# Performance work log

Measured on AMD Instinct MI355X. Metric: run time of the kernel, lower is better.

The kernel has to match this reference:

```python
import jax, jax.numpy as jnp
import numpy as np

FP4_VALUES = jnp.array([0.0, 0.5, 1.0, 1.5, 2.0, 3.0, 4.0, 6.0,
                        -0.0, -0.5, -1.0, -1.5, -2.0, -3.0, -4.0, -6.0], dtype=jnp.float32)
ALPHA = 1.702   # swiglu alpha
LIMIT = 7.0     # swiglu clamp limit
TOP_K = 4       # experts per token
EPS = 1e-5      # rmsnorm eps


def dequant_mxfp4(blocks, scales):
    """blocks: [E, R, G, B] int (uint8 values), scales: [E, R, G] int (E8M0 biased exp).
    Returns decoded weights [E, R, G*2B] fp32. Low nibble -> even cols, high nibble -> odd."""
    lo = FP4_VALUES[blocks & 15]
    hi = FP4_VALUES[(blocks >> 4) & 15]
    vals = jnp.stack([lo, hi], axis=-1).reshape(blocks.shape[:-1] + (-1,))  # [E,R,G,2B]
    w = jnp.ldexp(vals, (scales - 127)[..., None])
    return w.reshape(blocks.shape[:-2] + (-1,))


def rmsnorm(x, w):
    return x * jax.lax.rsqrt(jnp.mean(x * x, axis=-1, keepdims=True) + EPS) * w


def setup_inputs():
    key = jax.random.key(0)
    ks = jax.random.split(key, 10)
    E, H, I, B, S = 32, 1024, 1024, 1, 1024
    GB = 16  # packed bytes per 32-element group
    return {
        "x": jax.random.normal(ks[0], (B, S, H), jnp.float32),
        "norm_w": jnp.ones((H,), jnp.float32),
        "gate_w": jax.random.normal(ks[1], (E, H), jnp.float32) * 0.05,
        "gate_b": jax.random.normal(ks[2], (E,), jnp.float32) * 0.01,
        "mlp1_bias": jax.random.normal(ks[3], (E, 2 * I), jnp.float32) * 0.02,
        "mlp2_bias": jax.random.normal(ks[4], (E, H), jnp.float32) * 0.02,
        "mlp1_blocks": jax.random.randint(ks[5], (E, 2 * I, H // 32, GB), 0, 256, jnp.int32),
        "mlp1_scales": jax.random.randint(ks[6], (E, 2 * I, H // 32), 118, 125, jnp.int32),
        "mlp2_blocks": jax.random.randint(ks[7], (E, H, I // 32, GB), 0, 256, jnp.int32),
        "mlp2_scales": jax.random.randint(ks[8], (E, H, I // 32), 118, 125, jnp.int32),
    }


def reference(x, norm_w, gate_w, gate_b, mlp1_bias, mlp2_bias,
              mlp1_blocks, mlp1_scales, mlp2_blocks, mlp2_scales):
    B, S, H = x.shape
    N = B * S
    E = gate_w.shape[0]

    t = rmsnorm(x, norm_w).reshape(N, H)
    logits = t @ gate_w.T + gate_b                      # [N, E]
    top_vals, top_idx = jax.lax.top_k(logits, TOP_K)     # sorted descending, like torch.topk
    top_w = jax.nn.softmax(top_vals, axis=-1)            # [N, K]
    # dense routing matrix: nonzero only at selected experts (indices unique per token)
    route = jnp.zeros((N, E), x.dtype).at[jnp.arange(N)[:, None], top_idx].add(top_w)

    w1 = dequant_mxfp4(mlp1_blocks, mlp1_scales)         # [E, 2I, H]
    w2 = dequant_mxfp4(mlp2_blocks, mlp2_scales)         # [E, H, I]

    h = jnp.einsum('nh,eih->nei', t, w1) + mlp1_bias[None]  # [N, E, 2I]
    x_glu = jnp.minimum(h[..., 0::2], LIMIT)
    x_lin = jnp.clip(h[..., 1::2], -LIMIT, LIMIT)
    a = x_glu * jax.nn.sigmoid(ALPHA * x_glu) * (x_lin + 1.0)   # [N, E, I]
    y = jnp.einsum('nei,ehi->neh', a, w2) + mlp2_bias[None]      # [N, E, H]
    out = jnp.einsum('neh,ne->nh', y, route)                     # weighted combine
    return x + out.reshape(B, S, H)
```

## Files before the change

kernel.cpp:

```cpp
#include <hip/hip_runtime.h>
#include <hip/hip_bf16.h>
#include <math.h>


#define NE 32
#define HD 1024
#define ID 1024
#define NTOK 1024
#define R1 2048
#define TCH 160

typedef __attribute__((ext_vector_type(8)))  short bf16x8;
typedef __attribute__((ext_vector_type(16))) float f32x16;

#define TB_OFF   0
#define A_OFF    2097152
#define YB_OFF   10485760
#define CNT_OFF  18874368
#define OFFS_OFF 18874624
#define TOKL_OFF 18874880
#define TIDX_OFF 19005952
#define TWT_OFF  19022336
#define POS_OFF  19038720

__device__ __forceinline__ unsigned f2bf(float f) {
    unsigned u = __float_as_uint(f);
    return (u + 0x7FFFu + ((u >> 16) & 1u)) >> 16;
}
__device__ __forceinline__ float bf2f(unsigned u) {
    return __uint_as_float(u << 16);
}

__device__ __forceinline__ void dec8(int4 wv, unsigned dd, uint4& o) {
    unsigned u = __builtin_amdgcn_perm((unsigned)wv.y, (unsigned)wv.x, 0x00000400u);
    unsigned v = __builtin_amdgcn_perm((unsigned)wv.w, (unsigned)wv.z, 0x04000000u);
    unsigned packed = __builtin_amdgcn_perm(v, u, 0x07060100u);
    unsigned selE = packed & 0x07070707u;
    unsigned sE   = packed & 0x08080808u;
    unsigned ph   = packed >> 4;
    unsigned selO = ph & 0x07070707u;
    unsigned sO   = ph & 0x08080808u;
    const unsigned PH_hi = 0x40404040u, PH_lo = 0x3F3F3F14u;
    const unsigned PL_hi = 0xC0804000u, PL_lo = 0xC0800000u;
    unsigned hbE = __builtin_amdgcn_perm(PH_hi, PH_lo, selE) | (sE << 4);
    unsigned lbE = __builtin_amdgcn_perm(PL_hi, PL_lo, selE);
    unsigned hbO = __builtin_amdgcn_perm(PH_hi, PH_lo, selO) | (sO << 4);
    unsigned lbO = __builtin_amdgcn_perm(PL_hi, PL_lo, selO);
    unsigned mE0 = __builtin_amdgcn_perm(hbE, lbE, 0x05010400u);
    unsigned mE1 = __builtin_amdgcn_perm(hbE, lbE, 0x07030602u);
    unsigned mO0 = __builtin_amdgcn_perm(hbO, lbO, 0x05010400u);
    unsigned mO1 = __builtin_amdgcn_perm(hbO, lbO, 0x07030602u);
    unsigned r0 = __builtin_amdgcn_perm(mO0, mE0, 0x05040100u);
    unsigned r1 = __builtin_amdgcn_perm(mO0, mE0, 0x07060302u);
    unsigned r2 = __builtin_amdgcn_perm(mO1, mE1, 0x05040100u);
    unsigned r3 = __builtin_amdgcn_perm(mO1, mE1, 0x07060302u);
    unsigned o0, o1, o2, o3;
    asm("v_pk_add_u16 %0, %1, %2" : "=v"(o0) : "v"(r0), "v"(dd));
    asm("v_pk_add_u16 %0, %1, %2" : "=v"(o1) : "v"(r1), "v"(dd));
    asm("v_pk_add_u16 %0, %1, %2" : "=v"(o2) : "v"(r2), "v"(dd));
    asm("v_pk_add_u16 %0, %1, %2" : "=v"(o3) : "v"(r3), "v"(dd));
    o.x = o0; o.y = o1; o.z = o2; o.w = o3;
}

__global__ __launch_bounds__(256) void k_gate(
    const float* __restrict__ x, const float* __restrict__ norm_w,
    const float* __restrict__ gate_w, const float* __restrict__ gate_b,
    ushort* __restrict__ t_bf16, int* __restrict__ top_idx, float* __restrict__ top_wt)
{
    int n = blockIdx.x;
    int tid = threadIdx.x;
    __shared__ float tl[HD];
    __shared__ float red[4];
    __shared__ float logits[NE];

    const float4* xv = (const float4*)(x + (size_t)n * HD);
    float4 v = xv[tid];
    float ss = v.x * v.x + v.y * v.y + v.z * v.z + v.w * v.w;
    #pragma unroll
    for (int off = 32; off; off >>= 1) ss += __shfl_down(ss, off);
    if ((tid & 63) == 0) red[tid >> 6] = ss;
    __syncthreads();
    float tot = red[0] + red[1] + red[2] + red[3];
    float rms = rsqrtf(tot * (1.0f / HD) + 1e-5f);

    float4 w = ((const float4*)norm_w)[tid];
    float4 tv;
    tv.x = v.x * rms * w.x; tv.y = v.y * rms * w.y;
    tv.z = v.z * rms * w.z; tv.w = v.w * rms * w.w;
    ushort4 tb;
    tb.x = (ushort)f2bf(tv.x); tb.y = (ushort)f2bf(tv.y);
    tb.z = (ushort)f2bf(tv.z); tb.w = (ushort)f2bf(tv.w);
    ((ushort4*)(t_bf16 + (size_t)n * HD))[tid] = tb;
    ((float4*)tl)[tid] = tv;
    __syncthreads();

    int wv = tid >> 6, lane = tid & 63;
    for (int j = 0; j < 8; j++) {
        int e = wv * 8 + j;
        const float* gw = gate_w + (size_t)e * HD;
        float p = 0.f;
        #pragma unroll
        for (int q = 0; q < 16; q++) { int kk = lane + q * 64; p += tl[kk] * gw[kk]; }
        #pragma unroll
        for (int off = 32; off; off >>= 1) p += __shfl_down(p, off);
        if (lane == 0) logits[e] = p + gate_b[e];
    }
    __syncthreads();

    if (tid == 0) {
        float vals[4]; int idx[4];
        unsigned used = 0;
        #pragma unroll
        for (int kk = 0; kk < 4; kk++) {
            float best = -1e30f; int bi = 0;
            for (int e2 = 0; e2 < NE; e2++) {
                if (used & (1u << e2)) continue;
                if (logits[e2] > best) { best = logits[e2]; bi = e2; }
            }
            used |= 1u << bi; vals[kk] = best; idx[kk] = bi;
        }
        float m = vals[0], s = 0.f, ex[4];
        #pragma unroll
        for (int kk = 0; kk < 4; kk++) { ex[kk] = __expf(vals[kk] - m); s += ex[kk]; }
        float inv = 1.0f / s;
        #pragma unroll
        for (int kk = 0; kk < 4; kk++) {
            top_idx[n * 4 + kk] = idx[kk];
            top_wt[n * 4 + kk] = ex[kk] * inv;
        }
    }
}

__global__ void k_build(const int* __restrict__ top_idx, int* __restrict__ counts,
                        int* __restrict__ tok_list, int* __restrict__ pos_of)
{
    int i = blockIdx.x * 256 + threadIdx.x;
    if (i >= NTOK * 4) return;
    int n = i >> 2;
    int e = top_idx[i];
    int slot = atomicAdd(counts + e, 1);
    tok_list[e * NTOK + slot] = n;
    pos_of[i] = slot;
}

__global__ void k_prefix(const int* __restrict__ counts, int* __restrict__ offsets)
{
    if (threadIdx.x == 0) {
        int s = 0;
        for (int e = 0; e < NE; e++) { offsets[e] = s; s += counts[e]; }
        offsets[NE] = s;
    }
}

__global__ __launch_bounds__(256) void k_mlp1(
    const ushort* __restrict__ t_bf16, const int* __restrict__ blocks,
    const int* __restrict__ scales, const float* __restrict__ bias,
    const int* __restrict__ counts, const int* __restrict__ offsets,
    const int* __restrict__ tok_list, ushort* __restrict__ a)
{
    int e = blockIdx.y;
    int cnt = counts[e];
    if (cnt == 0) return;
    int r0 = blockIdx.x * 128;
    int tid = threadIdx.x;
    int w = tid >> 6, l = tid & 63;
    int base = offsets[e];

    __shared__ ushort tl[TCH][72];
    __shared__ ushort wl[128][72];
    __shared__ int tlist[TCH];

    int lrow = r0 + w * 32 + (l & 31);
    float b_lane = bias[e * R1 + lrow];
    int srow = tid >> 1, shalf = tid & 1;

    for (int c0 = 0; c0 < cnt; c0 += TCH) {
        int nt = min(TCH, cnt - c0);
        __syncthreads();
        if (tid < TCH) tlist[tid] = tok_list[e * NTOK + c0 + min(tid, nt - 1)];
        f32x16 acc[5] = {};

        #pragma unroll 1
        for (int k0 = 0; k0 < HD; k0 += 64) {
            __syncthreads();
            for (int idx = tid; idx < TCH * 8; idx += 256) {
                int tok = idx >> 3, seg = idx & 7;
                *(uint4*)&tl[tok][seg * 8] =
                    *(const uint4*)(t_bf16 + (size_t)tlist[tok] * HD + k0 + seg * 8);
            }
            {
                int g = (k0 >> 5) + shalf;
                size_t rbase = (size_t)(e * R1 + r0 + srow) * 32 + g;
                int s = scales[rbase];
                unsigned dd16 = (unsigned)((s - 127) << 7) & 0xFFFFu;
                unsigned dd = dd16 | (dd16 << 16);
                const int4* wp = (const int4*)(blocks + rbase * 16);
                ushort* dst = &wl[srow][shalf * 32];
                #pragma unroll
                for (int q = 0; q < 4; q++) {
                    uint4 ov;
                    dec8(wp[q], dd, ov);
                    *(uint4*)(dst + q * 8) = ov;
                }
            }
            __syncthreads();
            #pragma unroll
            for (int ks = 0; ks < 4; ks++) {
                bf16x8 wf = *(const bf16x8*)&wl[w * 32 + (l & 31)][ks * 16 + (l >> 5) * 8];
                #pragma unroll
                for (int mt = 0; mt < 5; mt++) {
                    bf16x8 af = *(const bf16x8*)&tl[mt * 32 + (l & 31)][ks * 16 + (l >> 5) * 8];
                    acc[mt] = __builtin_amdgcn_mfma_f32_32x32x16_bf16(af, wf, acc[mt], 0, 0, 0);
                }
            }
        }

        int p0 = (r0 + w * 32) >> 1;
        int pcol = p0 + ((l & 31) >> 1);
        #pragma unroll
        for (int mt = 0; mt < 5; mt++) {
            #pragma unroll
            for (int r = 0; r < 16; r++) {
                float h = acc[mt][r] + b_lane;
                float other = __shfl_xor(h, 1, 64);
                int m = (r & 3) + 8 * (r >> 2) + 4 * (l >> 5);
                int tokg = c0 + mt * 32 + m;
                if (!(l & 1) && tokg < cnt) {
                    float hg = fminf(h, 7.0f);
                    float hx = fminf(fmaxf(other, -7.0f), 7.0f);
                    float sig = 1.0f / (1.0f + __expf(-1.702f * hg));
                    float av = hg * sig * (hx + 1.0f);
                    a[(size_t)(base + tokg) * ID + pcol] = (ushort)f2bf(av);
                }
            }
        }
    }
}

__global__ __launch_bounds__(256) void k_mlp2(
    const ushort* __restrict__ a, const int* __restrict__ blocks,
    const int* __restrict__ scales, const float* __restrict__ bias,
    const int* __restrict__ counts, const int* __restrict__ offsets,
    ushort* __restrict__ yb)
{
    int e = blockIdx.y;
    int cnt = counts[e];
    if (cnt == 0) return;
    int r0 = blockIdx.x * 128;
    int tid = threadIdx.x;
    int w = tid >> 6, l = tid & 63;
    int base = offsets[e];

    __shared__ ushort tl[TCH][72];
    __shared__ ushort wl[128][72];

    int lrow = r0 + w * 32 + (l & 31);
    float b_lane = bias[e * HD + lrow];
    int srow = tid >> 1, shalf = tid & 1;

    for (int c0 = 0; c0 < cnt; c0 += TCH) {
        int nt = min(TCH, cnt - c0);
        f32x16 acc[5] = {};

        #pragma unroll 1
        for (int k0 = 0; k0 < ID; k0 += 64) {
            __syncthreads();
            for (int idx = tid; idx < TCH * 8; idx += 256) {
                int tok = idx >> 3, seg = idx & 7;
                int slot = base + c0 + min(tok, nt - 1);
                *(uint4*)&tl[tok][seg * 8] =
                    *(const uint4*)(a + (size_t)slot * ID + k0 + seg * 8);
            }
            {
                int g = (k0 >> 5) + shalf;
                size_t rbase = (size_t)(e * HD + r0 + srow) * 32 + g;
                int s = scales[rbase];
                unsigned dd16 = (unsigned)((s - 127) << 7) & 0xFFFFu;
                unsigned dd = dd16 | (dd16 << 16);
                const int4* wp = (const int4*)(blocks + rbase * 16);
                ushort* dst = &wl[srow][shalf * 32];
                #pragma unroll
                for (int q = 0; q < 4; q++) {
                    uint4 ov;
                    dec8(wp[q], dd, ov);
                    *(uint4*)(dst + q * 8) = ov;
                }
            }
            __syncthreads();
            #pragma unroll
            for (int ks = 0; ks < 4; ks++) {
                bf16x8 wf = *(const bf16x8*)&wl[w * 32 + (l & 31)][ks * 16 + (l >> 5) * 8];
                #pragma unroll
                for (int mt = 0; mt < 5; mt++) {
                    bf16x8 af = *(const bf16x8*)&tl[mt * 32 + (l & 31)][ks * 16 + (l >> 5) * 8];
                    acc[mt] = __builtin_amdgcn_mfma_f32_32x32x16_bf16(af, wf, acc[mt], 0, 0, 0);
                }
            }
        }

        int hcol = r0 + w * 32 + (l & 31);
        #pragma unroll
        for (int mt = 0; mt < 5; mt++) {
            #pragma unroll
            for (int r = 0; r < 16; r++) {
                int m = (r & 3) + 8 * (r >> 2) + 4 * (l >> 5);
                int tokg = c0 + mt * 32 + m;
                if (tokg < cnt) {
                    float y = acc[mt][r] + b_lane;
                    yb[(size_t)(base + tokg) * HD + hcol] = (ushort)f2bf(y);
                }
            }
        }
    }
}

__global__ __launch_bounds__(256) void k_combine(
    const float* __restrict__ x, const ushort* __restrict__ yb,
    const int* __restrict__ top_idx, const float* __restrict__ top_wt,
    const int* __restrict__ pos_of, const int* __restrict__ offsets,
    float* __restrict__ out)
{
    int n = blockIdx.x, tid = threadIdx.x;
    float4 xv = ((const float4*)(x + (size_t)n * HD))[tid];
    float r0 = xv.x, r1 = xv.y, r2 = xv.z, r3 = xv.w;
    #pragma unroll
    for (int k = 0; k < 4; k++) {
        int e = top_idx[n * 4 + k];
        float wt = top_wt[n * 4 + k];
        int slot = offsets[e] + pos_of[n * 4 + k];
        ushort4 yv = ((const ushort4*)(yb + (size_t)slot * HD))[tid];
        r0 += wt * bf2f(yv.x); r1 += wt * bf2f(yv.y);
        r2 += wt * bf2f(yv.z); r3 += wt * bf2f(yv.w);
    }
    float4 ov; ov.x = r0; ov.y = r1; ov.z = r2; ov.w = r3;
    ((float4*)(out + (size_t)n * HD))[tid] = ov;
}

extern "C" void kernel_launch(void* const* d_in, const int* in_sizes, int n_in,
                              void* d_out, int out_size, void* d_ws, size_t ws_size,
                              hipStream_t stream)
{
    const float* x           = (const float*)d_in[0];
    const float* norm_w      = (const float*)d_in[1];
    const float* gate_w      = (const float*)d_in[2];
    const float* gate_b      = (const float*)d_in[3];
    const float* mlp1_bias   = (const float*)d_in[4];
    const float* mlp2_bias   = (const float*)d_in[5];
    const int*   mlp1_blocks = (const int*)d_in[6];
    const int*   mlp1_scales = (const int*)d_in[7];
    const int*   mlp2_blocks = (const int*)d_in[8];
    const int*   mlp2_scales = (const int*)d_in[9];
    float* out = (float*)d_out;

    char* ws = (char*)d_ws;
    ushort* t_bf16  = (ushort*)(ws + TB_OFF);
    ushort* a       = (ushort*)(ws + A_OFF);
    ushort* yb      = (ushort*)(ws + YB_OFF);
    int*   counts   = (int*)(ws + CNT_OFF);
    int*   offsets  = (int*)(ws + OFFS_OFF);
    int*   tok_list = (int*)(ws + TOKL_OFF);
    int*   top_idx  = (int*)(ws + TIDX_OFF);
    float* top_wt   = (float*)(ws + TWT_OFF);
    int*   pos_of   = (int*)(ws + POS_OFF);

    hipMemsetAsync(counts, 0, NE * sizeof(int), stream);
    k_gate<<<NTOK, 256, 0, stream>>>(x, norm_w, gate_w, gate_b, t_bf16, top_idx, top_wt);
    k_build<<<(NTOK * 4 + 255) / 256, 256, 0, stream>>>(top_idx, counts, tok_list, pos_of);
    k_prefix<<<1, 64, 0, stream>>>(counts, offsets);
    k_mlp1<<<dim3(16, NE), 256, 0, stream>>>(t_bf16, mlp1_blocks, mlp1_scales, mlp1_bias,
                                             counts, offsets, tok_list, a);
    k_mlp2<<<dim3(8, NE), 256, 0, stream>>>(a, mlp2_blocks, mlp2_scales, mlp2_bias,
                                            counts, offsets, yb);
    k_combine<<<NTOK, 256, 0, stream>>>(x, yb, top_idx, top_wt, pos_of, offsets, out);
}
```

Measured before the change: 153.8 us.

## Repack MXFP4 weights, fold routing into gate, pipeline MLPs with direct-to-LDS loads

Adds a repack kernel that compacts the int32-stored fp4 blocks and scales into dense swizzled layouts each call. The gate kernel now assigns expert slots itself and scatters activations into a fixed per-expert, K-tiled layout, which removes the build and prefix kernels. Both MLP kernels are rewritten to use per-wave global_load_lds double buffering with manual waitcnt scheduling, register-held scales, 2x2 MFMA tiles and a split over token chunks via a grid z dimension. The repack pass adds traffic over the full weight set on every call, and the workspace grows considerably.

```diff
diff --git a/kernel.cpp b/kernel.cpp
--- a/kernel.cpp
+++ b/kernel.cpp
@@ -8,20 +8,23 @@
 #define ID 1024
 #define NTOK 1024
 #define R1 2048
-#define TCH 160
+#define SLOTS 32768
+#define TSTEP 4194304
 
 typedef __attribute__((ext_vector_type(8)))  short bf16x8;
 typedef __attribute__((ext_vector_type(16))) float f32x16;
 
-#define TB_OFF   0
-#define A_OFF    2097152
-#define YB_OFF   10485760
-#define CNT_OFF  18874368
-#define OFFS_OFF 18874624
-#define TOKL_OFF 18874880
-#define TIDX_OFF 19005952
-#define TWT_OFF  19022336
-#define POS_OFF  19038720
+#define WP1_OFF  0
+#define WP2_OFF  33554432
+#define SCT1_OFF 50331648
+#define SCT2_OFF 52428800
+#define TS_OFF   53477376
+#define AK_OFF   120586240
+#define YB_OFF   187695104
+#define CNT_OFF  254803968
+#define TIDX_OFF 254804224
+#define TWT_OFF  254820608
+#define POS_OFF  254836992
 
 __device__ __forceinline__ unsigned f2bf(float f) {
     unsigned u = __float_as_uint(f);
@@ -31,10 +34,7 @@
     return __uint_as_float(u << 16);
 }
 
-__device__ __forceinline__ void dec8(int4 wv, unsigned dd, uint4& o) {
-    unsigned u = __builtin_amdgcn_perm((unsigned)wv.y, (unsigned)wv.x, 0x00000400u);
-    unsigned v = __builtin_amdgcn_perm((unsigned)wv.w, (unsigned)wv.z, 0x04000000u);
-    unsigned packed = __builtin_amdgcn_perm(v, u, 0x07060100u);
+__device__ __forceinline__ bf16x8 dec8p(unsigned packed, unsigned dd) {
     unsigned selE = packed & 0x07070707u;
     unsigned sE   = packed & 0x08080808u;
     unsigned ph   = packed >> 4;
@@ -59,19 +59,103 @@
     asm("v_pk_add_u16 %0, %1, %2" : "=v"(o1) : "v"(r1), "v"(dd));
     asm("v_pk_add_u16 %0, %1, %2" : "=v"(o2) : "v"(r2), "v"(dd));
     asm("v_pk_add_u16 %0, %1, %2" : "=v"(o3) : "v"(r3), "v"(dd));
-    o.x = o0; o.y = o1; o.z = o2; o.w = o3;
+    uint4 o; o.x = o0; o.y = o1; o.z = o2; o.w = o3;
+    union { uint4 u4; bf16x8 b; } cv; cv.u4 = o;
+    return cv.b;
+}
+
+__device__ __forceinline__ void gll16(const void* g, void* l) {
+    __builtin_amdgcn_global_load_lds(
+        (const __attribute__((address_space(1))) unsigned int*)g,
+        (__attribute__((address_space(3))) unsigned int*)l, 16, 0, 0);
+}
+
+#define SB __builtin_amdgcn_sched_barrier(0)
+
+__device__ __forceinline__ unsigned sc_sel(uint4 a, uint4 b, int kt2) {
+    int idx = kt2 >> 1;
+    unsigned r0_ = (idx & 4) ? b.x : a.x;
+    unsigned r1_ = (idx & 4) ? b.y : a.y;
+    unsigned r2_ = (idx & 4) ? b.z : a.z;
+    unsigned r3_ = (idx & 4) ? b.w : a.w;
+    unsigned lo = (idx & 1) ? r1_ : r0_;
+    unsigned hi = (idx & 1) ? r3_ : r2_;
+    return (idx & 2) ? hi : lo;
+}
+
+__device__ __forceinline__ void repack_w_item(const int* __restrict__ blocks,
+                                              unsigned* __restrict__ wp, int rsh, int idx)
+{
+    int R = 1 << rsh;
+    int row = idx & (R - 1);
+    int ekt = idx >> rsh;
+    const int4* src = (const int4*)(blocks + ((size_t)(ekt >> 4) * R + row) * 512
+                                    + (ekt & 15) * 32);
+    unsigned d[8];
+    #pragma unroll
+    for (int q = 0; q < 8; q++) {
+        int4 v = src[q];
+        unsigned u = __builtin_amdgcn_perm((unsigned)v.y, (unsigned)v.x, 0x00000400u);
+        unsigned w = __builtin_amdgcn_perm((unsigned)v.w, (unsigned)v.z, 0x04000000u);
+        d[q] = __builtin_amdgcn_perm(w, u, 0x07060100u);
+    }
+    int r63 = row & 63;
+    int x = (r63 ^ (r63 >> 3)) & 7;
+    unsigned t;
+    if (x & 1) { t=d[0];d[0]=d[1];d[1]=t; t=d[2];d[2]=d[3];d[3]=t;
+                 t=d[4];d[4]=d[5];d[5]=t; t=d[6];d[6]=d[7];d[7]=t; }
+    if (x & 2) { t=d[0];d[0]=d[2];d[2]=t; t=d[1];d[1]=d[3];d[3]=t;
+                 t=d[4];d[4]=d[6];d[6]=t; t=d[5];d[5]=d[7];d[7]=t; }
+    if (x & 4) { t=d[0];d[0]=d[4];d[4]=t; t=d[1];d[1]=d[5];d[5]=t;
+                 t=d[2];d[2]=d[6];d[6]=t; t=d[3];d[3]=d[7];d[7]=t; }
+    uint4 o0; o0.x=d[0]; o0.y=d[1]; o0.z=d[2]; o0.w=d[3];
+    uint4 o1; o1.x=d[4]; o1.y=d[5]; o1.z=d[6]; o1.w=d[7];
+    *(uint4*)(wp + (size_t)idx * 8) = o0;
+    *(uint4*)(wp + (size_t)idx * 8 + 4) = o1;
+}
+
+__device__ __forceinline__ void repack_sc_item(const int* __restrict__ scales,
+                                               ushort* __restrict__ sct, int idx)
+{
+    const int* src = scales + (size_t)idx * 32;
+    unsigned o[8];
+    #pragma unroll
+    for (int d = 0; d < 8; d++) {
+        unsigned w0 = (src[4*d] & 0xFF) | ((src[4*d+1] & 0xFF) << 8);
+        unsigned w1 = (src[4*d+2] & 0xFF) | ((src[4*d+3] & 0xFF) << 8);
+        o[d] = w0 | (w1 << 16);
+    }
+    uint4 a; a.x=o[0]; a.y=o[1]; a.z=o[2]; a.w=o[3];
+    uint4 b; b.x=o[4]; b.y=o[5]; b.z=o[6]; b.w=o[7];
+    *(uint4*)(sct + (size_t)idx * 16) = a;
+    *(uint4*)(sct + (size_t)idx * 16 + 8) = b;
+}
+
+__global__ __launch_bounds__(256) void k_repack(
+    const int* __restrict__ b1, const int* __restrict__ b2,
+    const int* __restrict__ s1, const int* __restrict__ s2,
+    unsigned* __restrict__ wp1, unsigned* __restrict__ wp2,
+    ushort* __restrict__ sct1, ushort* __restrict__ sct2)
+{
+    int b = blockIdx.x, tid = threadIdx.x;
+    if (b < 4096)       repack_w_item(b1, wp1, 11, b * 256 + tid);
+    else if (b < 6144)  repack_w_item(b2, wp2, 10, (b - 4096) * 256 + tid);
+    else if (b < 6400)  repack_sc_item(s1, sct1, (b - 6144) * 256 + tid);
+    else                repack_sc_item(s2, sct2, (b - 6400) * 256 + tid);
 }
 
 __global__ __launch_bounds__(256) void k_gate(
     const float* __restrict__ x, const float* __restrict__ norm_w,
     const float* __restrict__ gate_w, const float* __restrict__ gate_b,
-    ushort* __restrict__ t_bf16, int* __restrict__ top_idx, float* __restrict__ top_wt)
+    ushort* __restrict__ t_s, int* __restrict__ top_idx, float* __restrict__ top_wt,
+    int* __restrict__ counts, int* __restrict__ pos_of)
 {
     int n = blockIdx.x;
     int tid = threadIdx.x;
     __shared__ float tl[HD];
     __shared__ float red[4];
     __shared__ float logits[NE];
+    __shared__ int s_se[4], s_sl[4];
 
     const float4* xv = (const float4*)(x + (size_t)n * HD);
     float4 v = xv[tid];
@@ -90,7 +174,6 @@
     ushort4 tb;
     tb.x = (ushort)f2bf(tv.x); tb.y = (ushort)f2bf(tv.y);
     tb.z = (ushort)f2bf(tv.z); tb.w = (ushort)f2bf(tv.w);
-    ((ushort4*)(t_bf16 + (size_t)n * HD))[tid] = tb;
     ((float4*)tl)[tid] = tv;
     __syncthreads();
 
@@ -127,198 +210,256 @@
         for (int kk = 0; kk < 4; kk++) {
             top_idx[n * 4 + kk] = idx[kk];
             top_wt[n * 4 + kk] = ex[kk] * inv;
+            int slot = atomicAdd(counts + idx[kk], 1);
+            pos_of[n * 4 + kk] = slot;
+            s_se[kk] = idx[kk]; s_sl[kk] = slot;
         }
     }
-}
-
-__global__ void k_build(const int* __restrict__ top_idx, int* __restrict__ counts,
-                        int* __restrict__ tok_list, int* __restrict__ pos_of)
-{
-    int i = blockIdx.x * 256 + threadIdx.x;
-    if (i >= NTOK * 4) return;
-    int n = i >> 2;
-    int e = top_idx[i];
-    int slot = atomicAdd(counts + e, 1);
-    tok_list[e * NTOK + slot] = n;
-    pos_of[i] = slot;
-}
-
-__global__ void k_prefix(const int* __restrict__ counts, int* __restrict__ offsets)
-{
-    if (threadIdx.x == 0) {
-        int s = 0;
-        for (int e = 0; e < NE; e++) { offsets[e] = s; s += counts[e]; }
-        offsets[NE] = s;
-    }
-}
-
-__global__ __launch_bounds__(256) void k_mlp1(
-    const ushort* __restrict__ t_bf16, const int* __restrict__ blocks,
-    const int* __restrict__ scales, const float* __restrict__ bias,
-    const int* __restrict__ counts, const int* __restrict__ offsets,
-    const int* __restrict__ tok_list, ushort* __restrict__ a)
+    __syncthreads();
+
+    int kt = tid >> 4, off = (tid & 15) * 4;
+    #pragma unroll
+    for (int kk = 0; kk < 4; kk++) {
+        int slot = (s_se[kk] << 10) + s_sl[kk];
+        *(ushort4*)&t_s[((size_t)kt * SLOTS + slot) * 64 + off] = tb;
+    }
+}
+
+#define M1_ISSUE(buf, kt) {                                                   \
+    const char* ws_ = wsrc + (size_t)(kt) * 65536;                            \
+    gll16(ws_, myw + (buf) * 2048);                                           \
+    gll16(ws_ + 1024, myw + (buf) * 2048 + 1024);                             \
+    const char* ts_ = tsrc + (size_t)(kt) * TSTEP;                            \
+    _Pragma("unroll")                                                         \
+    for (int i_ = 0; i_ < 8; i_++)                                            \
+        gll16(ts_ + i_ * 1024, myt + (buf) * 8192 + i_ * 1024);               \
+}
+
+#define M1_COMPUTE(buf, wordA, wordB) {                                       \
+    unsigned wa_ = (wordA), wb_ = (wordB);                                    \
+    unsigned dAl = (unsigned)(((int)(wa_ & 0xFF) - 127) << 7) & 0xFFFFu; dAl |= dAl << 16; \
+    unsigned dAh = (unsigned)(((int)((wa_ >> 8) & 0xFF) - 127) << 7) & 0xFFFFu; dAh |= dAh << 16; \
+    unsigned dBl = (unsigned)(((int)(wb_ & 0xFF) - 127) << 7) & 0xFFFFu; dBl |= dBl << 16; \
+    unsigned dBh = (unsigned)(((int)((wb_ >> 8) & 0xFF) - 127) << 7) & 0xFFFFu; dBh |= dBh << 16; \
+    _Pragma("unroll")                                                         \
+    for (int ks = 0; ks < 4; ks++) {                                          \
+        int s_ = ks * 2 + kh;                                                 \
+        unsigned w0_ = *(const unsigned*)(myw + (buf) * 2048 + lr * 32 + ((s_ ^ swz0) << 2)); \
+        unsigned w1_ = *(const unsigned*)(myw + (buf) * 2048 + (32 + lr) * 32 + ((s_ ^ swz1) << 2)); \
+        bf16x8 wf0 = dec8p(w0_, ks < 2 ? dAl : dAh);                          \
+        bf16x8 wf1 = dec8p(w1_, ks < 2 ? dBl : dBh);                          \
+        bf16x8 af0 = *(const bf16x8*)(myt + (buf) * 8192 + lr * 128 + ((s_ ^ (lr & 7)) << 4)); \
+        bf16x8 af1 = *(const bf16x8*)(myt + (buf) * 8192 + (32 + lr) * 128 + ((s_ ^ (lr & 7)) << 4)); \
+        a00 = __builtin_amdgcn_mfma_f32_32x32x16_bf16(af0, wf0, a00, 0, 0, 0); \
+        a01 = __builtin_amdgcn_mfma_f32_32x32x16_bf16(af1, wf0, a01, 0, 0, 0); \
+        a10 = __builtin_amdgcn_mfma_f32_32x32x16_bf16(af0, wf1, a10, 0, 0, 0); \
+        a11 = __builtin_amdgcn_mfma_f32_32x32x16_bf16(af1, wf1, a11, 0, 0, 0); \
+    }                                                                         \
+}
+
+#define M1_EPI(ac, nn, mt) {                                                  \
+    float bl = (nn) ? blB : blA;                                              \
+    int row_ = (nn) ? rowB : rowA;                                            \
+    int cc = (row_ >> 1) & 63;                                                \
+    _Pragma("unroll")                                                         \
+    for (int r = 0; r < 16; r++) {                                            \
+        float hv = ac[r] + bl;                                                \
+        float other = __shfl_xor(hv, 1, 64);                                  \
+        int m = (r & 3) + 8 * (r >> 2) + 4 * kh;                              \
+        int tokg = c0 + wt * 64 + (mt) * 32 + m;                              \
+        if (!(l & 1) && tokg < cnt) {                                         \
+            float hg = fminf(hv, 7.0f);                                       \
+            float hx = fminf(fmaxf(other, -7.0f), 7.0f);                      \
+            float sig = 1.0f / (1.0f + __expf(-1.702f * hg));                 \
+            float av = hg * sig * (hx + 1.0f);                                \
+            a_k[((size_t)g0 * SLOTS + sbase + tokg) * 64 + cc] = (ushort)f2bf(av); \
+        }                                                                     \
+    }                                                                         \
+}
+
+__global__ __launch_bounds__(256, 2) void k_mlp1(
+    const ushort* __restrict__ t_s, const unsigned* __restrict__ wp,
+    const ushort* __restrict__ sct, const float* __restrict__ bias,
+    const int* __restrict__ counts, ushort* __restrict__ a_k)
 {
     int e = blockIdx.y;
     int cnt = counts[e];
     if (cnt == 0) return;
+    int c00 = blockIdx.z * 128;
+    if (c00 >= cnt) return;
     int r0 = blockIdx.x * 128;
     int tid = threadIdx.x;
-    int w = tid >> 6, l = tid & 63;
-    int base = offsets[e];
-
-    __shared__ ushort tl[TCH][72];
-    __shared__ ushort wl[128][72];
-    __shared__ int tlist[TCH];
-
-    int lrow = r0 + w * 32 + (l & 31);
-    float b_lane = bias[e * R1 + lrow];
-    int srow = tid >> 1, shalf = tid & 1;
-
-    for (int c0 = 0; c0 < cnt; c0 += TCH) {
-        int nt = min(TCH, cnt - c0);
-        __syncthreads();
-        if (tid < TCH) tlist[tid] = tok_list[e * NTOK + c0 + min(tid, nt - 1)];
-        f32x16 acc[5] = {};
+    int l = tid & 63, lr = l & 31, kh = l >> 5;
+    int wu = __builtin_amdgcn_readfirstlane(tid >> 6);
+    int wr = wu >> 1, wt = wu & 1;
+    int sbase = e << 10;
+    int g0 = r0 >> 7;
+
+    __shared__ char lds_all[81920];
+    char* myt = lds_all + wu * 20480;
+    char* myw = myt + 16384;
+
+    int rowA = r0 + wr * 64 + lr, rowB = rowA + 32;
+    float blA = bias[e * R1 + rowA];
+    float blB = bias[e * R1 + rowB];
+    const uint4* spA = (const uint4*)(sct + (size_t)(e * R1 + rowA) * 16);
+    const uint4* spB = (const uint4*)(sct + (size_t)(e * R1 + rowB) * 16);
+    uint4 sA0 = spA[0], sA1 = spA[1];
+    uint4 sB0 = spB[0], sB1 = spB[1];
+    unsigned pin = sA0.x ^ sA0.y ^ sA0.z ^ sA0.w ^ sA1.x ^ sA1.y ^ sA1.z ^ sA1.w
+                 ^ sB0.x ^ sB0.y ^ sB0.z ^ sB0.w ^ sB1.x ^ sB1.y ^ sB1.z ^ sB1.w;
+    asm volatile("" :: "v"(pin), "v"(blA), "v"(blB));
+
+    const char* wsrc = (const char*)wp + (size_t)e * 16 * 65536
+                       + (size_t)(r0 + wr * 64) * 32 + (l >> 1) * 32 + (l & 1) * 16;
+    int tswz = ((l & 7) ^ (l >> 3)) << 4;
+    int swz0 = (lr ^ (lr >> 3)) & 7;
+    int swz1 = swz0 ^ 4;
+
+    #pragma unroll 1
+    for (int c0 = c00; c0 < cnt; c0 += 256) {
+        const char* tsrc = (const char*)t_s
+            + (size_t)(sbase + c0 + wt * 64 + (l >> 3)) * 128 + tswz;
+        asm volatile("s_waitcnt vmcnt(0)" ::: "memory"); SB;
+
+        f32x16 a00 = {}, a01 = {}, a10 = {}, a11 = {};
+        M1_ISSUE(0, 0); M1_ISSUE(1, 1); SB;
 
         #pragma unroll 1
-        for (int k0 = 0; k0 < HD; k0 += 64) {
-            __syncthreads();
-            for (int idx = tid; idx < TCH * 8; idx += 256) {
-                int tok = idx >> 3, seg = idx & 7;
-                *(uint4*)&tl[tok][seg * 8] =
-                    *(const uint4*)(t_bf16 + (size_t)tlist[tok] * HD + k0 + seg * 8);
-            }
-            {
-                int g = (k0 >> 5) + shalf;
-                size_t rbase = (size_t)(e * R1 + r0 + srow) * 32 + g;
-                int s = scales[rbase];
-                unsigned dd16 = (unsigned)((s - 127) << 7) & 0xFFFFu;
-                unsigned dd = dd16 | (dd16 << 16);
-                const int4* wp = (const int4*)(blocks + rbase * 16);
-                ushort* dst = &wl[srow][shalf * 32];
-                #pragma unroll
-                for (int q = 0; q < 4; q++) {
-                    uint4 ov;
-                    dec8(wp[q], dd, ov);
-                    *(uint4*)(dst + q * 8) = ov;
-                }
-            }
-            __syncthreads();
-            #pragma unroll
-            for (int ks = 0; ks < 4; ks++) {
-                bf16x8 wf = *(const bf16x8*)&wl[w * 32 + (l & 31)][ks * 16 + (l >> 5) * 8];
-                #pragma unroll
-                for (int mt = 0; mt < 5; mt++) {
-                    bf16x8 af = *(const bf16x8*)&tl[mt * 32 + (l & 31)][ks * 16 + (l >> 5) * 8];
-                    acc[mt] = __builtin_amdgcn_mfma_f32_32x32x16_bf16(af, wf, acc[mt], 0, 0, 0);
-                }
-            }
+        for (int kt2 = 0; kt2 < 16; kt2 += 2) {
+            unsigned dwA = sc_sel(sA0, sA1, kt2);
+            unsigned dwB = sc_sel(sB0, sB1, kt2);
+            asm volatile("s_waitcnt vmcnt(10)" ::: "memory"); SB;
+            M1_COMPUTE(0, dwA & 0xFFFFu, dwB & 0xFFFFu);
+            asm volatile("s_waitcnt lgkmcnt(0)" ::: "memory"); SB;
+            if (kt2 < 14) { M1_ISSUE(0, kt2 + 2); SB; }
+            if (kt2 < 14) { asm volatile("s_waitcnt vmcnt(10)" ::: "memory"); }
+            else          { asm volatile("s_waitcnt vmcnt(0)" ::: "memory"); }
+            SB;
+            M1_COMPUTE(1, dwA >> 16, dwB >> 16);
+            asm volatile("s_waitcnt lgkmcnt(0)" ::: "memory"); SB;
+            if (kt2 < 14) { M1_ISSUE(1, kt2 + 3); SB; }
         }
 
-        int p0 = (r0 + w * 32) >> 1;
-        int pcol = p0 + ((l & 31) >> 1);
-        #pragma unroll
-        for (int mt = 0; mt < 5; mt++) {
-            #pragma unroll
-            for (int r = 0; r < 16; r++) {
-                float h = acc[mt][r] + b_lane;
-                float other = __shfl_xor(h, 1, 64);
-                int m = (r & 3) + 8 * (r >> 2) + 4 * (l >> 5);
-                int tokg = c0 + mt * 32 + m;
-                if (!(l & 1) && tokg < cnt) {
-                    float hg = fminf(h, 7.0f);
-                    float hx = fminf(fmaxf(other, -7.0f), 7.0f);
-                    float sig = 1.0f / (1.0f + __expf(-1.702f * hg));
-                    float av = hg * sig * (hx + 1.0f);
-                    a[(size_t)(base + tokg) * ID + pcol] = (ushort)f2bf(av);
-                }
-            }
-        }
-    }
-}
-
-__global__ __launch_bounds__(256) void k_mlp2(
-    const ushort* __restrict__ a, const int* __restrict__ blocks,
-    const int* __restrict__ scales, const float* __restrict__ bias,
-    const int* __restrict__ counts, const int* __restrict__ offsets,
-    ushort* __restrict__ yb)
+        M1_EPI(a00, 0, 0); M1_EPI(a01, 0, 1);
+        M1_EPI(a10, 1, 0); M1_EPI(a11, 1, 1);
+    }
+}
+
+#define M2_ISSUE(buf, kt) {                                                   \
+    const char* ws_ = wsrc + (size_t)(kt) * 32768;                            \
+    gll16(ws_, myw + (buf) * 2048);                                           \
+    gll16(ws_ + 1024, myw + (buf) * 2048 + 1024);                             \
+    const char* ts_ = tsrc + (size_t)(kt) * TSTEP;                            \
+    _Pragma("unroll")                                                         \
+    for (int i_ = 0; i_ < 4; i_++)                                            \
+        gll16(ts_ + i_ * 1024, myt + (buf) * 4096 + i_ * 1024);               \
+}
+
+#define M2_COMPUTE(buf, wordA, wordB) {                                       \
+    unsigned wa_ = (wordA), wb_ = (wordB);                                    \
+    unsigned dAl = (unsigned)(((int)(wa_ & 0xFF) - 127) << 7) & 0xFFFFu; dAl |= dAl << 16; \
+    unsigned dAh = (unsigned)(((int)((wa_ >> 8) & 0xFF) - 127) << 7) & 0xFFFFu; dAh |= dAh << 16; \
+    unsigned dBl = (unsigned)(((int)(wb_ & 0xFF) - 127) << 7) & 0xFFFFu; dBl |= dBl << 16; \
+    unsigned dBh = (unsigned)(((int)((wb_ >> 8) & 0xFF) - 127) << 7) & 0xFFFFu; dBh |= dBh << 16; \
+    _Pragma("unroll")                                                         \
+    for (int ks = 0; ks < 4; ks++) {                                          \
+        int s_ = ks * 2 + kh;                                                 \
+        unsigned w0_ = *(const unsigned*)(myw + (buf) * 2048 + lr * 32 + ((s_ ^ swz0) << 2)); \
+        unsigned w1_ = *(const unsigned*)(myw + (buf) * 2048 + (32 + lr) * 32 + ((s_ ^ swz1) << 2)); \
+        bf16x8 wf0 = dec8p(w0_, ks < 2 ? dAl : dAh);                          \
+        bf16x8 wf1 = dec8p(w1_, ks < 2 ? dBl : dBh);                          \
+        bf16x8 af0 = *(const bf16x8*)(myt + (buf) * 4096 + lr * 128 + ((s_ ^ (lr & 7)) << 4)); \
+        a0 = __builtin_amdgcn_mfma_f32_32x32x16_bf16(af0, wf0, a0, 0, 0, 0);  \
+        a1 = __builtin_amdgcn_mfma_f32_32x32x16_bf16(af0, wf1, a1, 0, 0, 0);  \
+    }                                                                         \
+}
+
+#define M2_EPI(ac, nn) {                                                      \
+    float bl = (nn) ? blB : blA;                                              \
+    int row_ = (nn) ? rowB : rowA;                                            \
+    _Pragma("unroll")                                                         \
+    for (int r = 0; r < 16; r++) {                                            \
+        int m = (r & 3) + 8 * (r >> 2) + 4 * kh;                              \
+        int tokg = c0 + wt * 32 + m;                                          \
+        if (tokg < cnt) {                                                     \
+            float y = ac[r] + bl;                                             \
+            yb[(size_t)(sbase + tokg) * HD + row_] = (ushort)f2bf(y);         \
+        }                                                                     \
+    }                                                                         \
+}
+
+__global__ __launch_bounds__(256, 3) void k_mlp2(
+    const ushort* __restrict__ a_k, const unsigned* __restrict__ wp,
+    const ushort* __restrict__ sct, const float* __restrict__ bias,
+    const int* __restrict__ counts, ushort* __restrict__ yb)
 {
     int e = blockIdx.y;
     int cnt = counts[e];
     if (cnt == 0) return;
+    int c00 = blockIdx.z * 64;
+    if (c00 >= cnt) return;
     int r0 = blockIdx.x * 128;
     int tid = threadIdx.x;
-    int w = tid >> 6, l = tid & 63;
-    int base = offsets[e];
-
-    __shared__ ushort tl[TCH][72];
-    __shared__ ushort wl[128][72];
-
-    int lrow = r0 + w * 32 + (l & 31);
-    float b_lane = bias[e * HD + lrow];
-    int srow = tid >> 1, shalf = tid & 1;
-
-    for (int c0 = 0; c0 < cnt; c0 += TCH) {
-        int nt = min(TCH, cnt - c0);
-        f32x16 acc[5] = {};
+    int l = tid & 63, lr = l & 31, kh = l >> 5;
+    int wu = __builtin_amdgcn_readfirstlane(tid >> 6);
+    int wr = wu >> 1, wt = wu & 1;
+    int sbase = e << 10;
+
+    __shared__ char lds_all[49152];
+    char* myt = lds_all + wu * 12288;
+    char* myw = myt + 8192;
+
+    int rowA = r0 + wr * 64 + lr, rowB = rowA + 32;
+    float blA = bias[e * HD + rowA];
+    float blB = bias[e * HD + rowB];
+    const uint4* spA = (const uint4*)(sct + (size_t)(e * HD + rowA) * 16);
+    const uint4* spB = (const uint4*)(sct + (size_t)(e * HD + rowB) * 16);
+    uint4 sA0 = spA[0], sA1 = spA[1];
+    uint4 sB0 = spB[0], sB1 = spB[1];
+    unsigned pin = sA0.x ^ sA0.y ^ sA0.z ^ sA0.w ^ sA1.x ^ sA1.y ^ sA1.z ^ sA1.w
+                 ^ sB0.x ^ sB0.y ^ sB0.z ^ sB0.w ^ sB1.x ^ sB1.y ^ sB1.z ^ sB1.w;
+    asm volatile("" :: "v"(pin), "v"(blA), "v"(blB));
+
+    const char* wsrc = (const char*)wp + (size_t)e * 16 * 32768
+                       + (size_t)(r0 + wr * 64) * 32 + (l >> 1) * 32 + (l & 1) * 16;
+    int tswz = ((l & 7) ^ (l >> 3)) << 4;
+    int swz0 = (lr ^ (lr >> 3)) & 7;
+    int swz1 = swz0 ^ 4;
+
+    #pragma unroll 1
+    for (int c0 = c00; c0 < cnt; c0 += 192) {
+        const char* tsrc = (const char*)a_k
+            + (size_t)(sbase + c0 + wt * 32 + (l >> 3)) * 128 + tswz;
+        asm volatile("s_waitcnt vmcnt(0)" ::: "memory"); SB;
+
+        f32x16 a0 = {}, a1 = {};
+        M2_ISSUE(0, 0); M2_ISSUE(1, 1); SB;
 
         #pragma unroll 1
-        for (int k0 = 0; k0 < ID; k0 += 64) {
-            __syncthreads();
-            for (int idx = tid; idx < TCH * 8; idx += 256) {
-                int tok = idx >> 3, seg = idx & 7;
-                int slot = base + c0 + min(tok, nt - 1);
-                *(uint4*)&tl[tok][seg * 8] =
-                    *(const uint4*)(a + (size_t)slot * ID + k0 + seg * 8);
-            }
-            {
-                int g = (k0 >> 5) + shalf;
-                size_t rbase = (size_t)(e * HD + r0 + srow) * 32 + g;
-                int s = scales[rbase];
-                unsigned dd16 = (unsigned)((s - 127) << 7) & 0xFFFFu;
-                unsigned dd = dd16 | (dd16 << 16);
-                const int4* wp = (const int4*)(blocks + rbase * 16);
-                ushort* dst = &wl[srow][shalf * 32];
-                #pragma unroll
-                for (int q = 0; q < 4; q++) {
-                    uint4 ov;
-                    dec8(wp[q], dd, ov);
-                    *(uint4*)(dst + q * 8) = ov;
-                }
-            }
-            __syncthreads();
-            #pragma unroll
-            for (int ks = 0; ks < 4; ks++) {
-                bf16x8 wf = *(const bf16x8*)&wl[w * 32 + (l & 31)][ks * 16 + (l >> 5) * 8];
-                #pragma unroll
-                for (int mt = 0; mt < 5; mt++) {
-                    bf16x8 af = *(const bf16x8*)&tl[mt * 32 + (l & 31)][ks * 16 + (l >> 5) * 8];
-                    acc[mt] = __builtin_amdgcn_mfma_f32_32x32x16_bf16(af, wf, acc[mt], 0, 0, 0);
-                }
-            }
+        for (int kt2 = 0; kt2 < 16; kt2 += 2) {
+            unsigned dwA = sc_sel(sA0, sA1, kt2);
+            unsigned dwB = sc_sel(sB0, sB1, kt2);
+            asm volatile("s_waitcnt vmcnt(6)" ::: "memory"); SB;
+            M2_COMPUTE(0, dwA & 0xFFFFu, dwB & 0xFFFFu);
+            asm volatile("s_waitcnt lgkmcnt(0)" ::: "memory"); SB;
+            if (kt2 < 14) { M2_ISSUE(0, kt2 + 2); SB; }
+            if (kt2 < 14) { asm volatile("s_waitcnt vmcnt(6)" ::: "memory"); }
+            else          { asm volatile("s_waitcnt vmcnt(0)" ::: "memory"); }
+            SB;
+            M2_COMPUTE(1, dwA >> 16, dwB >> 16);
+            asm volatile("s_waitcnt lgkmcnt(0)" ::: "memory"); SB;
+            if (kt2 < 14) { M2_ISSUE(1, kt2 + 3); SB; }
         }
 
-        int hcol = r0 + w * 32 + (l & 31);
-        #pragma unroll
-        for (int mt = 0; mt < 5; mt++) {
-            #pragma unroll
-            for (int r = 0; r < 16; r++) {
-                int m = (r & 3) + 8 * (r >> 2) + 4 * (l >> 5);
-                int tokg = c0 + mt * 32 + m;
-                if (tokg < cnt) {
-                    float y = acc[mt][r] + b_lane;
-                    yb[(size_t)(base + tokg) * HD + hcol] = (ushort)f2bf(y);
-                }
-            }
-        }
+        M2_EPI(a0, 0); M2_EPI(a1, 1);
     }
 }
 
 __global__ __launch_bounds__(256) void k_combine(
     const float* __restrict__ x, const ushort* __restrict__ yb,
     const int* __restrict__ top_idx, const float* __restrict__ top_wt,
-    const int* __restrict__ pos_of, const int* __restrict__ offsets,
-    float* __restrict__ out)
+    const int* __restrict__ pos_of, float* __restrict__ out)
 {
     int n = blockIdx.x, tid = threadIdx.x;
     float4 xv = ((const float4*)(x + (size_t)n * HD))[tid];
@@ -327,7 +468,7 @@
     for (int k = 0; k < 4; k++) {
         int e = top_idx[n * 4 + k];
         float wt = top_wt[n * 4 + k];
-        int slot = offsets[e] + pos_of[n * 4 + k];
+        int slot = (e << 10) + pos_of[n * 4 + k];
         ushort4 yv = ((const ushort4*)(yb + (size_t)slot * HD))[tid];
         r0 += wt * bf2f(yv.x); r1 += wt * bf2f(yv.y);
         r2 += wt * bf2f(yv.z); r3 += wt * bf2f(yv.w);
@@ -353,23 +494,24 @@
     float* out = (float*)d_out;
 
     char* ws = (char*)d_ws;
-    ushort* t_bf16  = (ushort*)(ws + TB_OFF);
-    ushort* a       = (ushort*)(ws + A_OFF);
-    ushort* yb      = (ushort*)(ws + YB_OFF);
-    int*   counts   = (int*)(ws + CNT_OFF);
-    int*   offsets  = (int*)(ws + OFFS_OFF);
-    int*   tok_list = (int*)(ws + TOKL_OFF);
-    int*   top_idx  = (int*)(ws + TIDX_OFF);
-    float* top_wt   = (float*)(ws + TWT_OFF);
-    int*   pos_of   = (int*)(ws + POS_OFF);
+    unsigned* wp1  = (unsigned*)(ws + WP1_OFF);
+    unsigned* wp2  = (unsigned*)(ws + WP2_OFF);
+    ushort* sct1   = (ushort*)(ws + SCT1_OFF);
+    ushort* sct2   = (ushort*)(ws + SCT2_OFF);
+    ushort* t_s    = (ushort*)(ws + TS_OFF);
+    ushort* a_k    = (ushort*)(ws + AK_OFF);
+    ushort* yb     = (ushort*)(ws + YB_OFF);
+    int*   counts  = (int*)(ws + CNT_OFF);
+    int*   top_idx = (int*)(ws + TIDX_OFF);
+    float* top_wt  = (float*)(ws + TWT_OFF);
+    int*   pos_of  = (int*)(ws + POS_OFF);
 
     hipMemsetAsync(counts, 0, NE * sizeof(int), stream);
-    k_gate<<<NTOK, 256, 0, stream>>>(x, norm_w, gate_w, gate_b, t_bf16, top_idx, top_wt);
-    k_build<<<(NTOK * 4 + 255) / 256, 256, 0, stream>>>(top_idx, counts, tok_list, pos_of);
-    k_prefix<<<1, 64, 0, stream>>>(counts, offsets);
-    k_mlp1<<<dim3(16, NE), 256, 0, stream>>>(t_bf16, mlp1_blocks, mlp1_scales, mlp1_bias,
-                                             counts, offsets, tok_list, a);
-    k_mlp2<<<dim3(8, NE), 256, 0, stream>>>(a, mlp2_blocks, mlp2_scales, mlp2_bias,
-                                            counts, offsets, yb);
-    k_combine<<<NTOK, 256, 0, stream>>>(x, yb, top_idx, top_wt, pos_of, offsets, out);
-}
+    k_repack<<<6528, 256, 0, stream>>>(mlp1_blocks, mlp2_blocks, mlp1_scales, mlp2_scales,
+                                       wp1, wp2, sct1, sct2);
+    k_gate<<<NTOK, 256, 0, stream>>>(x, norm_w, gate_w, gate_b, t_s, top_idx, top_wt,
+                                     counts, pos_of);
+    k_mlp1<<<dim3(16, NE, 2), 256, 0, stream>>>(t_s, wp1, sct1, mlp1_bias, counts, a_k);
+    k_mlp2<<<dim3(8, NE, 3), 256, 0, stream>>>(a_k, wp2, sct2, mlp2_bias, counts, yb);
+    k_combine<<<NTOK, 256, 0, stream>>>(x, yb, top_idx, top_wt, pos_of, out);
+}
```

Result: slower. 178.4 us (+16.0%).
